# Kernel optimization log

Measured on AMD Instinct MI355X. Metric: run time of the kernel, lower is better.

## Reference

```python
import jax, jax.numpy as jnp
import numpy as np

VOC, EDIM, HDIM, SSZ, SDIM, SDEPTH, PAD = 32000, 256, 256, 128, 128, 2, 0
N, BSZ = 64, 32
T = 2 * N - 1  # 127
N_ACTS = 2  # push, pop


def _linear(key, out_d, in_d):
    k1, k2 = jax.random.split(key)
    return (jax.random.normal(k1, (out_d, in_d), jnp.float32) * 0.02,
            jax.random.normal(k2, (out_d,), jnp.float32) * 0.02)


def setup_inputs() -> dict:
    key = jax.random.key(0)
    ks = jax.random.split(key, 9)
    emb_W = jax.random.normal(ks[0], (VOC, EDIM), jnp.float32) * 0.02
    emb_W = emb_W.at[PAD].set(0.0)  # padding_idx row is zero in torch
    W_e2h, b_e2h = _linear(ks[1], HDIM, EDIM)
    W_s2h, b_s2h = _linear(ks[2], HDIM, SDIM * SDEPTH)
    W_h2h, b_h2h = _linear(ks[3], HDIM, HDIM)
    W_h2i, b_h2i = _linear(ks[4], N_ACTS + 1, HDIM)
    W_h2s, b_h2s = _linear(ks[5], SDIM, HDIM)
    W_s2u, b_s2u = _linear(ks[6], SDIM, SDIM * SDEPTH)
    empty_elem = jax.random.normal(ks[7], (1, SDIM), jnp.float32) * 0.02
    inputs = jax.random.randint(ks[8], (N, BSZ), 0, VOC)
    return dict(inputs=inputs, emb_W=emb_W, W_e2h=W_e2h, b_e2h=b_e2h,
                W_s2h=W_s2h, b_s2h=b_s2h, W_h2h=W_h2h, b_h2h=b_h2h,
                W_h2i=W_h2i, b_h2i=b_h2i, W_h2s=W_h2s, b_h2s=b_h2s,
                W_s2u=W_s2u, b_s2u=b_s2u, empty_elem=empty_elem)


def _srnn(inputs, emb_W, W_e2h, b_e2h, W_s2h, b_s2h, W_h2h, b_h2h,
          W_h2i, b_h2i, W_h2s, b_h2s, W_s2u, b_s2u, empty_elem):
    bsz = inputs.shape[1]
    embs = emb_W[inputs]                                        # [N, bsz, edim]
    pads = jnp.broadcast_to(emb_W[PAD], (T - N, bsz, EDIM))     # padded tail
    buf0 = jnp.concatenate([embs, pads], axis=0)                # [T, bsz, edim]
    hid0 = jnp.zeros((bsz, HDIM), jnp.float32)
    stack0 = jnp.broadcast_to(empty_elem, (bsz, SSZ, SDIM))

    def step(carry, t):
        hid, stack, buf = carry
        tops = stack[:, :SDEPTH, :].reshape(bsz, SDEPTH * SDIM)
        inp = buf[t]                                            # [bsz, edim]
        ihid = inp @ W_e2h.T + b_e2h + tops @ W_s2h.T + b_s2h
        hid = jax.nn.relu(hid @ W_h2h.T + b_h2h + ihid)
        inst = ihid @ W_h2i.T + b_h2i                           # [bsz, 3]
        act = jax.nn.softmax(inst[:, :N_ACTS], axis=-1)
        gamma = 1.0 + jnp.log1p(jnp.exp(inst[:, N_ACTS:]))      # [bsz, 1]
        a = act ** gamma
        a = a / (jnp.sum(a, axis=-1, keepdims=True) + 1e-16)    # sharpened acts
        p_push, p_pop = a[:, :1], a[:, 1:]                      # [bsz, 1]
        # buffer update: pop shifts the whole buffer down one slot along time
        buf_pop = jnp.concatenate([jnp.zeros_like(buf[:1]), buf[:-1]], axis=0)
        buf = p_push[None] * buf + p_pop[None] * buf_pop        # [1,bsz,1] bcast
        push_val = jax.nn.relu(hid @ W_h2s.T + b_h2s)           # [bsz, sdim]
        u_val = jax.nn.relu(tops @ W_s2u.T + b_s2u)             # [bsz, sdim]
        z = jnp.zeros((bsz, 1, SDIM), jnp.float32)
        # W_push (shift down by 1) as an index roll
        stack_push = jnp.concatenate([z, stack[:, :-1, :]], axis=1)
        stack_push = stack_push.at[:, 0, :].add(push_val)
        # W_pop = shift up by SDEPTH, then W_push = shift down by 1
        up = jnp.concatenate([stack[:, SDEPTH:, :],
                              jnp.zeros((bsz, SDEPTH, SDIM), jnp.float32)], axis=1)
        stack_pop = jnp.concatenate([z, up[:, :-1, :]], axis=1)
        stack_pop = stack_pop.at[:, 0, :].add(u_val)
        stack_pop = stack_pop.at[:, SSZ - SDEPTH + 1:, :].add(empty_elem[0])
        stack = p_push[:, :, None] * stack_push + p_pop[:, :, None] * stack_pop
        return (hid, stack, buf), (hid, a, stack[:, 0, :])

    (hid, stack, _), (outputs, acts, top_elems) = jax.lax.scan(
        step, (hid0, stack0, buf0), jnp.arange(T))
    return outputs, hid, stack, acts, top_elems


def reference(inputs, emb_W, W_e2h, b_e2h, W_s2h, b_s2h, W_h2h, b_h2h,
              W_h2i, b_h2i, W_h2s, b_h2s, W_s2u, b_s2u, empty_elem):
    return _srnn(inputs, emb_W, W_e2h, b_e2h, W_s2h, b_s2h, W_h2h, b_h2h,
                 W_h2i, b_h2i, W_h2s, b_h2s, W_s2u, b_s2u, empty_elem)
```

## Files before the change

kernel.cpp:

```cpp
#include <hip/hip_runtime.h>
#include <stdint.h>
#include <math.h>


#define T_STEPS 127

#define OUT_OFF   0
#define HID_OFF   1040384
#define STACK_OFF 1048576
#define ACTS_OFF  1572864
#define TE_OFF    1580992

#define E2H_OFF_U 131072

typedef _Float16 h2 __attribute__((ext_vector_type(2)));

__device__ __forceinline__ unsigned packh2(float a, float b){
  h2 v; v.x = (_Float16)a; v.y = (_Float16)b;
  return __builtin_bit_cast(unsigned, v);
}
__device__ __forceinline__ float h2loF(unsigned u){ h2 v = __builtin_bit_cast(h2,u); return (float)v.x; }
__device__ __forceinline__ float h2hiF(unsigned u){ h2 v = __builtin_bit_cast(h2,u); return (float)v.y; }

#if __has_builtin(__builtin_amdgcn_fdot2)
__device__ __forceinline__ float fdot2(unsigned a, unsigned b, float c){
  return __builtin_amdgcn_fdot2(__builtin_bit_cast(h2,a), __builtin_bit_cast(h2,b), c, false);
}
#else
__device__ __forceinline__ float fdot2(unsigned a, unsigned b, float c){
  return c + h2loF(a)*h2loF(b) + h2hiF(a)*h2hiF(b);
}
#endif

#define CHOFF(u) (12*((u)>>3) + ((u)&7))

__global__ void prep_pack(const float* __restrict__ We2h, const float* __restrict__ Ws2h,
                          const float* __restrict__ Wh2h, const float* __restrict__ Wh2s,
                          const float* __restrict__ Ws2u, uint4* __restrict__ out4){
  int gid = blockIdx.x*256 + threadIdx.x;
  const float* src;
  if (gid < 16384){
    int i = gid >> 10, t_ = gid & 1023;
    const float* S = (t_ < 512) ? Ws2h : Wh2h;
    int r = t_ & 511, jp = r >> 2, ks = r & 3;
    int j = 2*jp + (i >> 3);
    int k0 = ks*64 + (i & 7)*8;
    src = S + j*256 + k0;
  } else if (gid < 20480){
    int l = gid - 16384, i = l >> 10, t_ = l & 1023;
    int jr = t_ >> 4, kb = t_ & 15;
    int j = 2*jr + (i >> 1);
    int k0 = kb*16 + (i & 1)*8;
    src = Wh2s + j*256 + k0;
  } else if (gid < 24576){
    int l = gid - 20480, i = l >> 10, t_ = l & 1023;
    int jr = t_ >> 4, kb = t_ & 15;
    int j = 2*jr + (i >> 1);
    int k0 = kb*16 + (i & 1)*8;
    src = Ws2u + j*256 + k0;
  } else {
    int l = gid - 24576;
    int i8 = l >> 8, j = l & 255;
    src = We2h + j*256 + i8*8;
  }
  uint4 r4;
  r4.x = packh2(src[0], src[1]); r4.y = packh2(src[2], src[3]);
  r4.z = packh2(src[4], src[5]); r4.w = packh2(src[6], src[7]);
  out4[gid] = r4;
}

__global__ void prep_e2h(const int* __restrict__ inputs, const float* __restrict__ embW,
                         const uint4* __restrict__ w04, unsigned* __restrict__ e2hpk){
  __shared__ float emb[8][256];
  int tid = threadIdx.x;
  int r2 = blockIdx.x >> 3, bg = blockIdx.x & 7;
  for (int q=0;q<8;q++){
    int rr = q >> 2, bb = q & 3;
    int tok = inputs[(2*r2+rr)*32 + bg*4+bb];
    emb[q][tid] = embW[tok*256 + tid];
  }
  __syncthreads();
  float acc[8] = {0.f,0.f,0.f,0.f,0.f,0.f,0.f,0.f};
  for (int i8=0;i8<32;i8++){
    uint4 u = w04[i8*256 + tid];
    unsigned uu[4] = {u.x,u.y,u.z,u.w};
    #pragma unroll
    for (int c=0;c<4;c++){
      float lo = h2loF(uu[c]), hi = h2hiF(uu[c]);
      int k = i8*8 + c*2;
      #pragma unroll
      for (int q=0;q<8;q++)
        acc[q] += emb[q][k]*lo + emb[q][k+1]*hi;
    }
  }
  int base = (bg*4)*8192 + r2*256 + tid;
  #pragma unroll
  for (int bb=0;bb<4;bb++)
    e2hpk[base + bb*8192] = packh2(acc[bb], acc[4+bb]);
}

__global__ __attribute__((amdgpu_flat_work_group_size(1024,1024), amdgpu_waves_per_eu(4,4)))
void srnn_main(const uint4* __restrict__ ws4, const unsigned* __restrict__ wsu,
               const float* __restrict__ b_e2h, const float* __restrict__ b_s2h,
               const float* __restrict__ b_h2h, const float* __restrict__ Wh2i,
               const float* __restrict__ b_h2i, const float* __restrict__ b_h2s,
               const float* __restrict__ b_s2u, const float* __restrict__ empty_el,
               float* __restrict__ out)
{
  __shared__ __align__(16) float    stk_s[128*128];
  __shared__ __align__(16) unsigned e2h_s[32*258];
  __shared__ __align__(16) unsigned s_pk[192];
  __shared__ __align__(16) unsigned hid_pk[192];
  __shared__ __align__(16) float    pv_s[128], uv_s[128];
  __shared__ __align__(16) float    accih[256], acchp[256];
  __shared__ __align__(16) float    emptyf_s[128];
  __shared__ float    wbuf[2][192];
  __shared__ unsigned pkwc[32];
  __shared__ float    partsum[12];
  __shared__ float    pp_s, pq_s;

  const int tid = threadIdx.x;
  const int b   = blockIdx.x;
  const int aside = tid >> 9;
  const int ar  = tid & 511;
  const int ajp = ar >> 2;
  const int aks = ar & 3;
  const int jr  = tid >> 4;
  const int ksb = tid & 15;
  const int g   = tid >> 6;
  const int cp  = tid & 63;

  uint4 w1r[16], w3r[4], w2r[4];
  #pragma unroll
  for (int i=0;i<16;i++) w1r[i] = ws4[i*1024 + tid];
  #pragma unroll
  for (int i=0;i<4;i++)  w3r[i] = ws4[16384 + i*1024 + tid];
  #pragma unroll
  for (int i=0;i<4;i++)  w2r[i] = ws4[20480 + i*1024 + tid];

  float bA0=0.f, bA1=0.f;
  if (aks==0){
    int j0 = 2*ajp;
    if (aside==0){ bA0 = b_e2h[j0]+b_s2h[j0]; bA1 = b_e2h[j0+1]+b_s2h[j0+1]; }
    else         { bA0 = b_h2h[j0];           bA1 = b_h2h[j0+1]; }
  }
  float bH0=0.f,bH1=0.f,bU0=0.f,bU1=0.f;
  if (ksb==0){ bH0=b_h2s[2*jr]; bH1=b_h2s[2*jr+1]; bU0=b_s2u[2*jr]; bU1=b_s2u[2*jr+1]; }
  float rW0=0.f,rW1=0.f,rW2=0.f;
  if (tid<256){ rW0=Wh2i[tid]; rW1=Wh2i[256+tid]; rW2=Wh2i[512+tid]; }
  const float bi0=b_h2i[0], bi1=b_h2i[1], bi2=b_h2i[2];

  const unsigned* e2hg = wsu + E2H_OFF_U + b*8192;
  #pragma unroll
  for (int q=0;q<8;q++){
    int idx = q*1024 + tid;
    e2h_s[(idx>>8)*258 + (idx&255)] = e2hg[idx];
  }
  {
    float2 e2 = *(const float2*)&empty_el[2*cp];
    #pragma unroll
    for (int j=0;j<8;j++)
      *(float2*)&stk_s[(8*g+j)*128 + 2*cp] = e2;
  }
  if (tid < 128){
    emptyf_s[tid] = empty_el[tid];
    hid_pk[CHOFF(tid)] = 0u;
    int cu = tid & 63;
    s_pk[CHOFF(tid)] = packh2(empty_el[2*cu], empty_el[2*cu+1]);
  }
  if (tid < 192){ wbuf[0][tid] = (tid==64)?1.f:0.f; wbuf[1][tid]=0.f; }
  if (tid < 32)  pkwc[tid] = (tid==0)? packh2(1.f,0.f) : 0u;
  __syncthreads();

  int cur = 0;
  for (int t=0;t<T_STEPS;++t){
    {
      const unsigned* act  = aside ? hid_pk : s_pk;
      const unsigned* actB = act + 48*aks;
      float x0 = 0.f, x1 = 0.f;
      if (aside==0){
        #pragma unroll
        for (int q=0;q<8;q++){
          int r2 = aks*8 + q;
          unsigned cw = pkwc[r2];
          uint2 e = *(const uint2*)&e2h_s[r2*258 + 2*ajp];
          x0 = fdot2(cw, e.x, x0);
          x1 = fdot2(cw, e.y, x1);
        }
      }
      #pragma unroll
      for (int i=0;i<8;i++){
        uint4 A  = *(const uint4*)(actB + 12*(i>>1) + 4*(i&1));
        uint4 Wa = w1r[i], Wb = w1r[8+i];
        x0 = fdot2(A.x,Wa.x,x0); x0 = fdot2(A.y,Wa.y,x0);
        x0 = fdot2(A.z,Wa.z,x0); x0 = fdot2(A.w,Wa.w,x0);
        x1 = fdot2(A.x,Wb.x,x1); x1 = fdot2(A.y,Wb.y,x1);
        x1 = fdot2(A.z,Wb.z,x1); x1 = fdot2(A.w,Wb.w,x1);
      }
      x0 += __shfl_xor(x0,1); x0 += __shfl_xor(x0,2);
      x1 += __shfl_xor(x1,1); x1 += __shfl_xor(x1,2);
      if (aks==0){
        float* dst = aside ? acchp : accih;
        *(float2*)&dst[2*ajp] = make_float2(x0 + bA0, x1 + bA1);
      }
    }
    __syncthreads();

    if (tid < 128){
      float2 ih2 = *(const float2*)&accih[2*tid];
      float2 hp2 = *(const float2*)&acchp[2*tid];
      float hn0 = fmaxf(ih2.x+hp2.x, 0.f);
      float hn1 = fmaxf(ih2.y+hp2.y, 0.f);
      hid_pk[CHOFF(tid)] = packh2(hn0,hn1);
      *(float2*)&out[OUT_OFF + t*8192 + b*256 + 2*tid] = make_float2(hn0,hn1);
      if (t==T_STEPS-1) *(float2*)&out[HID_OFF + b*256 + 2*tid] = make_float2(hn0,hn1);
    }
    if (tid < 256){
      float v = accih[tid];
      float p0=v*rW0, p1=v*rW1, p2=v*rW2;
      #pragma unroll
      for (int o=32;o>=1;o>>=1){ p0+=__shfl_xor(p0,o); p1+=__shfl_xor(p1,o); p2+=__shfl_xor(p2,o); }
      if ((tid&63)==0){ int w=tid>>6; partsum[w*3]=p0; partsum[w*3+1]=p1; partsum[w*3+2]=p2; }
    }
    __syncthreads();

    if (tid < 64){
      float i0 = bi0+partsum[0]+partsum[3]+partsum[6]+partsum[9];
      float i1 = bi1+partsum[1]+partsum[4]+partsum[7]+partsum[10];
      float gi = bi2+partsum[2]+partsum[5]+partsum[8]+partsum[11];
      float mx = fmaxf(i0,i1);
      float e0 = expf(i0-mx), e1 = expf(i1-mx);
      float inv = 1.f/(e0+e1);
      float act0 = e0*inv, act1 = e1*inv;
      float gamma = 1.f + log1pf(expf(gi));
      float A0 = powf(act0,gamma), A1 = powf(act1,gamma);
      float sden = A0+A1+1e-16f;
      float ppv = A0/sden, pqv = A1/sden;
      if (tid==0){
        pp_s = ppv; pq_s = pqv;
        *(float2*)&out[ACTS_OFF + t*64 + b*2] = make_float2(ppv,pqv);
      }
    }

    {
      const uint4* hptr = (const uint4*)(hid_pk + 12*ksb);
      const uint4* sptr = (const uint4*)(s_pk   + 12*ksb);
      uint4 H0 = hptr[0], H1 = hptr[1];
      uint4 S0 = sptr[0], S1 = sptr[1];
      float h0=0.f,h1=0.f,u0=0.f,u1=0.f;
      h0=fdot2(H0.x,w3r[0].x,h0); h0=fdot2(H0.y,w3r[0].y,h0); h0=fdot2(H0.z,w3r[0].z,h0); h0=fdot2(H0.w,w3r[0].w,h0);
      h0=fdot2(H1.x,w3r[1].x,h0); h0=fdot2(H1.y,w3r[1].y,h0); h0=fdot2(H1.z,w3r[1].z,h0); h0=fdot2(H1.w,w3r[1].w,h0);
      h1=fdot2(H0.x,w3r[2].x,h1); h1=fdot2(H0.y,w3r[2].y,h1); h1=fdot2(H0.z,w3r[2].z,h1); h1=fdot2(H0.w,w3r[2].w,h1);
      h1=fdot2(H1.x,w3r[3].x,h1); h1=fdot2(H1.y,w3r[3].y,h1); h1=fdot2(H1.z,w3r[3].z,h1); h1=fdot2(H1.w,w3r[3].w,h1);
      u0=fdot2(S0.x,w2r[0].x,u0); u0=fdot2(S0.y,w2r[0].y,u0); u0=fdot2(S0.z,w2r[0].z,u0); u0=fdot2(S0.w,w2r[0].w,u0);
      u0=fdot2(S1.x,w2r[1].x,u0); u0=fdot2(S1.y,w2r[1].y,u0); u0=fdot2(S1.z,w2r[1].z,u0); u0=fdot2(S1.w,w2r[1].w,u0);
      u1=fdot2(S0.x,w2r[2].x,u1); u1=fdot2(S0.y,w2r[2].y,u1); u1=fdot2(S0.z,w2r[2].z,u1); u1=fdot2(S0.w,w2r[2].w,u1);
      u1=fdot2(S1.x,w2r[3].x,u1); u1=fdot2(S1.y,w2r[3].y,u1); u1=fdot2(S1.z,w2r[3].z,u1); u1=fdot2(S1.w,w2r[3].w,u1);
      #pragma unroll
      for (int o=8;o>=1;o>>=1){
        h0+=__shfl_xor(h0,o); h1+=__shfl_xor(h1,o);
        u0+=__shfl_xor(u0,o); u1+=__shfl_xor(u1,o);
      }
      if (ksb==0){
        pv_s[2*jr]   = fmaxf(h0+bH0,0.f);
        pv_s[2*jr+1] = fmaxf(h1+bH1,0.f);
        uv_s[2*jr]   = fmaxf(u0+bU0,0.f);
        uv_s[2*jr+1] = fmaxf(u1+bU1,0.f);
      }
    }
    __syncthreads();
    const float pp = pp_s, pq = pq_s;

    {
      float2 w[10];
      #pragma unroll
      for (int k=0;k<10;k++){
        int r = 8*g - 1 + k;
        if (r >= 0 && r <= 127)
          w[k] = *(const float2*)&stk_s[r*128 + 2*cp];
      }
      if (g == 15) w[9] = *(const float2*)&emptyf_s[2*cp];
      float2 pv2 = make_float2(0.f,0.f), uv2 = make_float2(0.f,0.f);
      if (g == 0){ pv2 = *(const float2*)&pv_s[2*cp]; uv2 = *(const float2*)&uv_s[2*cp]; }
      float2 nn[8];
      #pragma unroll
      for (int j=0;j<8;j++){
        nn[j].x = pp*w[j].x + pq*w[j+2].x;
        nn[j].y = pp*w[j].y + pq*w[j+2].y;
      }
      if (g == 0){
        nn[0].x = pp*pv2.x + pq*uv2.x;
        nn[0].y = pp*pv2.y + pq*uv2.y;
      }
      if (tid < 128){
        int k = 64+tid;
        wbuf[cur^1][k] = pp*wbuf[cur][k] + pq*wbuf[cur][k-1];
      } else if (tid < 160){
        int r2 = tid-128;
        int k1 = 65 + t - 2*r2;
        float wa = wbuf[cur][k1], wb2 = wbuf[cur][k1-1], wc2 = wbuf[cur][k1-2];
        pkwc[r2] = packh2(pp*wa+pq*wb2, pp*wb2+pq*wc2);
      }
      __syncthreads();
      #pragma unroll
      for (int j=0;j<8;j++)
        *(float2*)&stk_s[(8*g+j)*128 + 2*cp] = nn[j];
      if (g == 0){
        *(float2*)&out[TE_OFF + t*4096 + b*128 + 2*cp] = nn[0];
        s_pk[CHOFF(cp)]      = packh2(nn[0].x, nn[0].y);
        s_pk[CHOFF(64+cp)]   = packh2(nn[1].x, nn[1].y);
      }
    }
    __syncthreads();
    cur ^= 1;
  }

  #pragma unroll
  for (int j=0;j<8;j++){
    int r = 8*g + j;
    *(float2*)&out[STACK_OFF + b*16384 + r*128 + 2*cp] =
      *(const float2*)&stk_s[r*128 + 2*cp];
  }
}

extern "C" void kernel_launch(void* const* d_in, const int* in_sizes, int n_in,
                              void* d_out, int out_size, void* d_ws, size_t ws_size,
                              hipStream_t stream){
  const int*   inputs = (const int*)d_in[0];
  const float* embW   = (const float*)d_in[1];
  const float* We2h   = (const float*)d_in[2];
  const float* b_e2h  = (const float*)d_in[3];
  const float* Ws2h   = (const float*)d_in[4];
  const float* b_s2h  = (const float*)d_in[5];
  const float* Wh2h   = (const float*)d_in[6];
  const float* b_h2h  = (const float*)d_in[7];
  const float* Wh2i   = (const float*)d_in[8];
  const float* b_h2i  = (const float*)d_in[9];
  const float* Wh2s   = (const float*)d_in[10];
  const float* b_h2s  = (const float*)d_in[11];
  const float* Ws2u   = (const float*)d_in[12];
  const float* b_s2u  = (const float*)d_in[13];
  const float* empty  = (const float*)d_in[14];
  unsigned* wsu = (unsigned*)d_ws;

  prep_pack<<<dim3(128), dim3(256), 0, stream>>>(We2h, Ws2h, Wh2h, Wh2s, Ws2u, (uint4*)wsu);
  prep_e2h<<<dim3(256), dim3(256), 0, stream>>>(inputs, embW, ((const uint4*)wsu)+24576, wsu + E2H_OFF_U);
  srnn_main<<<dim3(32), dim3(1024), 0, stream>>>((const uint4*)wsu, (const unsigned*)wsu,
                                                 b_e2h, b_s2h, b_h2h, Wh2i, b_h2i,
                                                 b_h2s, b_s2u, empty, (float*)d_out);
}
```

Measured before the change: 892.0 us.

## Cut per-step barriers via halo double-buffering and fused stack projections

Merges the two prep kernels into one launch, with the e2h projection reading fp32 We2h directly. In the recurrent loop, the stack update now writes in place by keeping double-buffered halo rows for the rows just above and below each group. This removes the barrier between reading and writing the stack. The h2s/s2u projections are split across two halves of the block and use the freshly computed hidden state directly from the pre-activation sums. That lets them run in the same phase as the hidden update and removes another barrier per step. The trade-offs are more shared memory, some redundant relu/pack work, and a more complex indexing scheme.

```diff
diff --git a/kernel.cpp b/kernel.cpp
--- a/kernel.cpp
+++ b/kernel.cpp
@@ -11,6 +11,8 @@
 #define ACTS_OFF  1572864
 #define TE_OFF    1580992
 
+#define W3_OFF 16384
+#define W2_OFF 20480
 #define E2H_OFF_U 131072
 
 typedef _Float16 h2 __attribute__((ext_vector_type(2)));
@@ -33,47 +35,42 @@
 #endif
 
 #define CHOFF(u) (12*((u)>>3) + ((u)&7))
-
-__global__ void prep_pack(const float* __restrict__ We2h, const float* __restrict__ Ws2h,
-                          const float* __restrict__ Wh2h, const float* __restrict__ Wh2s,
-                          const float* __restrict__ Ws2u, uint4* __restrict__ out4){
-  int gid = blockIdx.x*256 + threadIdx.x;
-  const float* src;
-  if (gid < 16384){
-    int i = gid >> 10, t_ = gid & 1023;
-    const float* S = (t_ < 512) ? Ws2h : Wh2h;
-    int r = t_ & 511, jp = r >> 2, ks = r & 3;
-    int j = 2*jp + (i >> 3);
-    int k0 = ks*64 + (i & 7)*8;
-    src = S + j*256 + k0;
-  } else if (gid < 20480){
-    int l = gid - 16384, i = l >> 10, t_ = l & 1023;
-    int jr = t_ >> 4, kb = t_ & 15;
-    int j = 2*jr + (i >> 1);
-    int k0 = kb*16 + (i & 1)*8;
-    src = Wh2s + j*256 + k0;
-  } else if (gid < 24576){
-    int l = gid - 20480, i = l >> 10, t_ = l & 1023;
-    int jr = t_ >> 4, kb = t_ & 15;
-    int j = 2*jr + (i >> 1);
-    int k0 = kb*16 + (i & 1)*8;
-    src = Ws2u + j*256 + k0;
-  } else {
-    int l = gid - 24576;
-    int i8 = l >> 8, j = l & 255;
-    src = We2h + j*256 + i8*8;
-  }
-  uint4 r4;
-  r4.x = packh2(src[0], src[1]); r4.y = packh2(src[2], src[3]);
-  r4.z = packh2(src[4], src[5]); r4.w = packh2(src[6], src[7]);
-  out4[gid] = r4;
-}
-
-__global__ void prep_e2h(const int* __restrict__ inputs, const float* __restrict__ embW,
-                         const uint4* __restrict__ w04, unsigned* __restrict__ e2hpk){
+#define STGP(p)  (20*((p)>>3) + 2*((p)&7))
+
+__global__ void prep_all(const int* __restrict__ inputs, const float* __restrict__ embW,
+                         const float* __restrict__ We2h,
+                         const float* __restrict__ Ws2h, const float* __restrict__ Wh2h,
+                         const float* __restrict__ Wh2s, const float* __restrict__ Ws2u,
+                         uint4* __restrict__ out4, unsigned* __restrict__ e2hpk){
+  int tid = threadIdx.x;
+  int bi  = blockIdx.x;
+  if (bi >= 256){
+    int gid = (bi-256)*256 + tid;
+    const float* src;
+    if (gid < 16384){
+      int i = gid >> 10, t_ = gid & 1023;
+      const float* S = (t_ < 512) ? Ws2h : Wh2h;
+      int r = t_ & 511, jp = r >> 2, ks = r & 3;
+      int j  = 2*jp + (i >> 3);
+      int k0 = ks*64 + (i & 7)*8;
+      src = S + j*256 + k0;
+    } else {
+      int l = gid - 16384;
+      int region = l >> 12, li = l & 4095;
+      int i = li >> 9, rB = li & 511;
+      int jp = rB >> 3, ks = rB & 7;
+      int j  = 2*jp + (i >> 2);
+      int k0 = ks*32 + (i & 3)*8;
+      src = (region ? Ws2u : Wh2s) + j*256 + k0;
+    }
+    uint4 r4;
+    r4.x = packh2(src[0], src[1]); r4.y = packh2(src[2], src[3]);
+    r4.z = packh2(src[4], src[5]); r4.w = packh2(src[6], src[7]);
+    out4[gid] = r4;
+    return;
+  }
   __shared__ float emb[8][256];
-  int tid = threadIdx.x;
-  int r2 = blockIdx.x >> 3, bg = blockIdx.x & 7;
+  int r2 = bi >> 3, bg = bi & 7;
   for (int q=0;q<8;q++){
     int rr = q >> 2, bb = q & 3;
     int tok = inputs[(2*r2+rr)*32 + bg*4+bb];
@@ -82,11 +79,12 @@
   __syncthreads();
   float acc[8] = {0.f,0.f,0.f,0.f,0.f,0.f,0.f,0.f};
   for (int i8=0;i8<32;i8++){
-    uint4 u = w04[i8*256 + tid];
-    unsigned uu[4] = {u.x,u.y,u.z,u.w};
+    float4 f0 = *(const float4*)&We2h[tid*256 + i8*8];
+    float4 f1 = *(const float4*)&We2h[tid*256 + i8*8 + 4];
+    float wv[8] = {f0.x,f0.y,f0.z,f0.w,f1.x,f1.y,f1.z,f1.w};
     #pragma unroll
     for (int c=0;c<4;c++){
-      float lo = h2loF(uu[c]), hi = h2hiF(uu[c]);
+      float lo = wv[2*c], hi = wv[2*c+1];
       int k = i8*8 + c*2;
       #pragma unroll
       for (int q=0;q<8;q++)
@@ -108,15 +106,15 @@
                float* __restrict__ out)
 {
   __shared__ __align__(16) float    stk_s[128*128];
-  __shared__ __align__(16) unsigned e2h_s[32*258];
-  __shared__ __align__(16) unsigned s_pk[192];
-  __shared__ __align__(16) unsigned hid_pk[192];
+  __shared__ __align__(16) unsigned e2h4[16*520];
+  __shared__ __align__(16) float    halo_top[2][16*128];
+  __shared__ __align__(16) float    halo_bot[2][16*128];
+  __shared__ __align__(16) float    accih_st[320], acchp_st[320];
+  __shared__ __align__(16) unsigned s_pk[192], hid_pk[192];
   __shared__ __align__(16) float    pv_s[128], uv_s[128];
-  __shared__ __align__(16) float    accih[256], acchp[256];
-  __shared__ __align__(16) float    emptyf_s[128];
+  __shared__ __align__(16) float    whi_s[768];
   __shared__ float    wbuf[2][192];
   __shared__ unsigned pkwc[32];
-  __shared__ float    partsum[12];
   __shared__ float    pp_s, pq_s;
 
   const int tid = threadIdx.x;
@@ -125,18 +123,21 @@
   const int ar  = tid & 511;
   const int ajp = ar >> 2;
   const int aks = ar & 3;
-  const int jr  = tid >> 4;
-  const int ksb = tid & 15;
+  const int rB  = tid & 511;
+  const int jpB = rB >> 3;
+  const int ksB = rB & 7;
+  const int h2sSide = (tid >= 512);
   const int g   = tid >> 6;
   const int cp  = tid & 63;
 
-  uint4 w1r[16], w3r[4], w2r[4];
+  uint4 w1r[16], wBr[8];
   #pragma unroll
   for (int i=0;i<16;i++) w1r[i] = ws4[i*1024 + tid];
-  #pragma unroll
-  for (int i=0;i<4;i++)  w3r[i] = ws4[16384 + i*1024 + tid];
-  #pragma unroll
-  for (int i=0;i<4;i++)  w2r[i] = ws4[20480 + i*1024 + tid];
+  {
+    int wbase = h2sSide ? W3_OFF : W2_OFF;
+    #pragma unroll
+    for (int i=0;i<8;i++) wBr[i] = ws4[wbase + i*512 + rB];
+  }
 
   float bA0=0.f, bA1=0.f;
   if (aks==0){
@@ -144,26 +145,28 @@
     if (aside==0){ bA0 = b_e2h[j0]+b_s2h[j0]; bA1 = b_e2h[j0+1]+b_s2h[j0+1]; }
     else         { bA0 = b_h2h[j0];           bA1 = b_h2h[j0+1]; }
   }
-  float bH0=0.f,bH1=0.f,bU0=0.f,bU1=0.f;
-  if (ksb==0){ bH0=b_h2s[2*jr]; bH1=b_h2s[2*jr+1]; bU0=b_s2u[2*jr]; bU1=b_s2u[2*jr+1]; }
-  float rW0=0.f,rW1=0.f,rW2=0.f;
-  if (tid<256){ rW0=Wh2i[tid]; rW1=Wh2i[256+tid]; rW2=Wh2i[512+tid]; }
+  float bB0=0.f, bB1=0.f;
+  if (ksB==0){
+    const float* bb = h2sSide ? b_h2s : b_s2u;
+    bB0 = bb[2*jpB]; bB1 = bb[2*jpB+1];
+  }
   const float bi0=b_h2i[0], bi1=b_h2i[1], bi2=b_h2i[2];
 
   const unsigned* e2hg = wsu + E2H_OFF_U + b*8192;
   #pragma unroll
   for (int q=0;q<8;q++){
     int idx = q*1024 + tid;
-    e2h_s[(idx>>8)*258 + (idx&255)] = e2hg[idx];
-  }
-  {
-    float2 e2 = *(const float2*)&empty_el[2*cp];
-    #pragma unroll
-    for (int j=0;j<8;j++)
-      *(float2*)&stk_s[(8*g+j)*128 + 2*cp] = e2;
-  }
+    int r2 = idx >> 8, j = idx & 255;
+    e2h4[(r2>>1)*520 + 2*j + (r2&1)] = e2hg[idx];
+  }
+  const float2 emt2 = *(const float2*)&empty_el[2*cp];
+  #pragma unroll
+  for (int j=0;j<8;j++)
+    *(float2*)&stk_s[(8*g+j)*128 + 2*cp] = emt2;
+  *(float2*)&halo_top[0][g*128 + 2*cp] = emt2;
+  *(float2*)&halo_bot[0][g*128 + 2*cp] = emt2;
+  if (tid < 768) whi_s[tid] = Wh2i[tid];
   if (tid < 128){
-    emptyf_s[tid] = empty_el[tid];
     hid_pk[CHOFF(tid)] = 0u;
     int cu = tid & 63;
     s_pk[CHOFF(tid)] = packh2(empty_el[2*cu], empty_el[2*cu+1]);
@@ -180,12 +183,13 @@
       float x0 = 0.f, x1 = 0.f;
       if (aside==0){
         #pragma unroll
-        for (int q=0;q<8;q++){
-          int r2 = aks*8 + q;
-          unsigned cw = pkwc[r2];
-          uint2 e = *(const uint2*)&e2h_s[r2*258 + 2*ajp];
-          x0 = fdot2(cw, e.x, x0);
-          x1 = fdot2(cw, e.y, x1);
+        for (int qq=0;qq<4;qq++){
+          int r2g = 4*aks + qq;
+          unsigned cwE = pkwc[8*aks + 2*qq];
+          unsigned cwO = pkwc[8*aks + 2*qq + 1];
+          uint4 u = *(const uint4*)&e2h4[r2g*520 + 4*ajp];
+          x0 = fdot2(cwE, u.x, x0); x0 = fdot2(cwO, u.y, x0);
+          x1 = fdot2(cwE, u.z, x1); x1 = fdot2(cwO, u.w, x1);
         }
       }
       #pragma unroll
@@ -200,34 +204,70 @@
       x0 += __shfl_xor(x0,1); x0 += __shfl_xor(x0,2);
       x1 += __shfl_xor(x1,1); x1 += __shfl_xor(x1,2);
       if (aks==0){
-        float* dst = aside ? acchp : accih;
-        *(float2*)&dst[2*ajp] = make_float2(x0 + bA0, x1 + bA1);
+        float* dst = aside ? acchp_st : accih_st;
+        *(float2*)&dst[STGP(ajp)] = make_float2(x0 + bA0, x1 + bA1);
       }
     }
     __syncthreads();
 
-    if (tid < 128){
-      float2 ih2 = *(const float2*)&accih[2*tid];
-      float2 hp2 = *(const float2*)&acchp[2*tid];
+    if (tid >= 64 && tid < 192){
+      int hl = tid - 64;
+      int w_ = STGP(hl);
+      float2 ih2 = *(const float2*)&accih_st[w_];
+      float2 hp2 = *(const float2*)&acchp_st[w_];
       float hn0 = fmaxf(ih2.x+hp2.x, 0.f);
       float hn1 = fmaxf(ih2.y+hp2.y, 0.f);
-      hid_pk[CHOFF(tid)] = packh2(hn0,hn1);
-      *(float2*)&out[OUT_OFF + t*8192 + b*256 + 2*tid] = make_float2(hn0,hn1);
-      if (t==T_STEPS-1) *(float2*)&out[HID_OFF + b*256 + 2*tid] = make_float2(hn0,hn1);
-    }
-    if (tid < 256){
-      float v = accih[tid];
-      float p0=v*rW0, p1=v*rW1, p2=v*rW2;
-      #pragma unroll
-      for (int o=32;o>=1;o>>=1){ p0+=__shfl_xor(p0,o); p1+=__shfl_xor(p1,o); p2+=__shfl_xor(p2,o); }
-      if ((tid&63)==0){ int w=tid>>6; partsum[w*3]=p0; partsum[w*3+1]=p1; partsum[w*3+2]=p2; }
-    }
-    __syncthreads();
+      hid_pk[CHOFF(hl)] = packh2(hn0,hn1);
+      *(float2*)&out[OUT_OFF + t*8192 + b*256 + 2*hl] = make_float2(hn0,hn1);
+      if (t==T_STEPS-1) *(float2*)&out[HID_OFF + b*256 + 2*hl] = make_float2(hn0,hn1);
+    }
+
+    {
+      float y0=0.f, y1=0.f;
+      #pragma unroll
+      for (int i=0;i<4;i++){
+        unsigned u0,u1,u2,u3;
+        if (h2sSide){
+          const int off = 40*ksB + ((i>=2)?20:0) + 8*(i&1);
+          float4 a0 = *(const float4*)(accih_st + off);
+          float4 a1 = *(const float4*)(accih_st + off + 4);
+          float4 c0 = *(const float4*)(acchp_st + off);
+          float4 c1 = *(const float4*)(acchp_st + off + 4);
+          u0 = packh2(fmaxf(a0.x+c0.x,0.f), fmaxf(a0.y+c0.y,0.f));
+          u1 = packh2(fmaxf(a0.z+c0.z,0.f), fmaxf(a0.w+c0.w,0.f));
+          u2 = packh2(fmaxf(a1.x+c1.x,0.f), fmaxf(a1.y+c1.y,0.f));
+          u3 = packh2(fmaxf(a1.z+c1.z,0.f), fmaxf(a1.w+c1.w,0.f));
+        } else {
+          uint4 S = *(const uint4*)&s_pk[12*(2*ksB + (i>>1)) + 4*(i&1)];
+          u0 = S.x; u1 = S.y; u2 = S.z; u3 = S.w;
+        }
+        uint4 Wa = wBr[i], Wb = wBr[4+i];
+        y0=fdot2(u0,Wa.x,y0); y0=fdot2(u1,Wa.y,y0); y0=fdot2(u2,Wa.z,y0); y0=fdot2(u3,Wa.w,y0);
+        y1=fdot2(u0,Wb.x,y1); y1=fdot2(u1,Wb.y,y1); y1=fdot2(u2,Wb.z,y1); y1=fdot2(u3,Wb.w,y1);
+      }
+      y0 += __shfl_xor(y0,1); y0 += __shfl_xor(y0,2); y0 += __shfl_xor(y0,4);
+      y1 += __shfl_xor(y1,1); y1 += __shfl_xor(y1,2); y1 += __shfl_xor(y1,4);
+      if (ksB==0){
+        float* dst = h2sSide ? pv_s : uv_s;
+        dst[2*jpB]   = fmaxf(y0+bB0,0.f);
+        dst[2*jpB+1] = fmaxf(y1+bB1,0.f);
+      }
+    }
 
     if (tid < 64){
-      float i0 = bi0+partsum[0]+partsum[3]+partsum[6]+partsum[9];
-      float i1 = bi1+partsum[1]+partsum[4]+partsum[7]+partsum[10];
-      float gi = bi2+partsum[2]+partsum[5]+partsum[8]+partsum[11];
+      int l = tid;
+      float4 av = *(const float4*)&accih_st[20*(l>>2) + 4*(l&3)];
+      float4 q0 = *(const float4*)&whi_s[4*l];
+      float4 q1 = *(const float4*)&whi_s[256 + 4*l];
+      float4 q2 = *(const float4*)&whi_s[512 + 4*l];
+      float p0 = av.x*q0.x + av.y*q0.y + av.z*q0.z + av.w*q0.w;
+      float p1 = av.x*q1.x + av.y*q1.y + av.z*q1.z + av.w*q1.w;
+      float p2 = av.x*q2.x + av.y*q2.y + av.z*q2.z + av.w*q2.w;
+      #pragma unroll
+      for (int o=1;o<=32;o<<=1){
+        p0 += __shfl_xor(p0,o); p1 += __shfl_xor(p1,o); p2 += __shfl_xor(p2,o);
+      }
+      float i0 = bi0+p0, i1 = bi1+p1, gi = bi2+p2;
       float mx = fmaxf(i0,i1);
       float e0 = expf(i0-mx), e1 = expf(i1-mx);
       float inv = 1.f/(e0+e1);
@@ -235,62 +275,45 @@
       float gamma = 1.f + log1pf(expf(gi));
       float A0 = powf(act0,gamma), A1 = powf(act1,gamma);
       float sden = A0+A1+1e-16f;
-      float ppv = A0/sden, pqv = A1/sden;
-      if (tid==0){
+      if (l==0){
+        float ppv = A0/sden, pqv = A1/sden;
         pp_s = ppv; pq_s = pqv;
         *(float2*)&out[ACTS_OFF + t*64 + b*2] = make_float2(ppv,pqv);
       }
     }
-
-    {
-      const uint4* hptr = (const uint4*)(hid_pk + 12*ksb);
-      const uint4* sptr = (const uint4*)(s_pk   + 12*ksb);
-      uint4 H0 = hptr[0], H1 = hptr[1];
-      uint4 S0 = sptr[0], S1 = sptr[1];
-      float h0=0.f,h1=0.f,u0=0.f,u1=0.f;
-      h0=fdot2(H0.x,w3r[0].x,h0); h0=fdot2(H0.y,w3r[0].y,h0); h0=fdot2(H0.z,w3r[0].z,h0); h0=fdot2(H0.w,w3r[0].w,h0);
-      h0=fdot2(H1.x,w3r[1].x,h0); h0=fdot2(H1.y,w3r[1].y,h0); h0=fdot2(H1.z,w3r[1].z,h0); h0=fdot2(H1.w,w3r[1].w,h0);
-      h1=fdot2(H0.x,w3r[2].x,h1); h1=fdot2(H0.y,w3r[2].y,h1); h1=fdot2(H0.z,w3r[2].z,h1); h1=fdot2(H0.w,w3r[2].w,h1);
-      h1=fdot2(H1.x,w3r[3].x,h1); h1=fdot2(H1.y,w3r[3].y,h1); h1=fdot2(H1.z,w3r[3].z,h1); h1=fdot2(H1.w,w3r[3].w,h1);
-      u0=fdot2(S0.x,w2r[0].x,u0); u0=fdot2(S0.y,w2r[0].y,u0); u0=fdot2(S0.z,w2r[0].z,u0); u0=fdot2(S0.w,w2r[0].w,u0);
-      u0=fdot2(S1.x,w2r[1].x,u0); u0=fdot2(S1.y,w2r[1].y,u0); u0=fdot2(S1.z,w2r[1].z,u0); u0=fdot2(S1.w,w2r[1].w,u0);
-      u1=fdot2(S0.x,w2r[2].x,u1); u1=fdot2(S0.y,w2r[2].y,u1); u1=fdot2(S0.z,w2r[2].z,u1); u1=fdot2(S0.w,w2r[2].w,u1);
-      u1=fdot2(S1.x,w2r[3].x,u1); u1=fdot2(S1.y,w2r[3].y,u1); u1=fdot2(S1.z,w2r[3].z,u1); u1=fdot2(S1.w,w2r[3].w,u1);
-      #pragma unroll
-      for (int o=8;o>=1;o>>=1){
-        h0+=__shfl_xor(h0,o); h1+=__shfl_xor(h1,o);
-        u0+=__shfl_xor(u0,o); u1+=__shfl_xor(u1,o);
-      }
-      if (ksb==0){
-        pv_s[2*jr]   = fmaxf(h0+bH0,0.f);
-        pv_s[2*jr+1] = fmaxf(h1+bH1,0.f);
-        uv_s[2*jr]   = fmaxf(u0+bU0,0.f);
-        uv_s[2*jr+1] = fmaxf(u1+bU1,0.f);
-      }
-    }
     __syncthreads();
     const float pp = pp_s, pq = pq_s;
 
     {
       float2 w[10];
       #pragma unroll
-      for (int k=0;k<10;k++){
-        int r = 8*g - 1 + k;
-        if (r >= 0 && r <= 127)
-          w[k] = *(const float2*)&stk_s[r*128 + 2*cp];
-      }
-      if (g == 15) w[9] = *(const float2*)&emptyf_s[2*cp];
+      for (int k=1;k<=8;k++)
+        w[k] = *(const float2*)&stk_s[(8*g + k - 1)*128 + 2*cp];
+      w[0] = (g>0)  ? *(const float2*)&halo_bot[cur][(g-1)*128 + 2*cp]
+                    : make_float2(0.f,0.f);
+      w[9] = (g<15) ? *(const float2*)&halo_top[cur][(g+1)*128 + 2*cp]
+                    : emt2;
       float2 pv2 = make_float2(0.f,0.f), uv2 = make_float2(0.f,0.f);
       if (g == 0){ pv2 = *(const float2*)&pv_s[2*cp]; uv2 = *(const float2*)&uv_s[2*cp]; }
-      float2 nn[8];
+      float2 nn0, nn1;
       #pragma unroll
       for (int j=0;j<8;j++){
-        nn[j].x = pp*w[j].x + pq*w[j+2].x;
-        nn[j].y = pp*w[j].y + pq*w[j+2].y;
+        float2 nv;
+        nv.x = pp*w[j].x + pq*w[j+2].x;
+        nv.y = pp*w[j].y + pq*w[j+2].y;
+        if (j==0 && g==0){
+          nv.x = pp*pv2.x + pq*uv2.x;
+          nv.y = pp*pv2.y + pq*uv2.y;
+        }
+        *(float2*)&stk_s[(8*g+j)*128 + 2*cp] = nv;
+        if (j==0){ nn0 = nv; *(float2*)&halo_top[cur^1][g*128 + 2*cp] = nv; }
+        if (j==1){ nn1 = nv; }
+        if (j==7){ *(float2*)&halo_bot[cur^1][g*128 + 2*cp] = nv; }
       }
       if (g == 0){
-        nn[0].x = pp*pv2.x + pq*uv2.x;
-        nn[0].y = pp*pv2.y + pq*uv2.y;
+        *(float2*)&out[TE_OFF + t*4096 + b*128 + 2*cp] = nn0;
+        s_pk[CHOFF(cp)]    = packh2(nn0.x, nn0.y);
+        s_pk[CHOFF(64+cp)] = packh2(nn1.x, nn1.y);
       }
       if (tid < 128){
         int k = 64+tid;
@@ -301,26 +324,15 @@
         float wa = wbuf[cur][k1], wb2 = wbuf[cur][k1-1], wc2 = wbuf[cur][k1-2];
         pkwc[r2] = packh2(pp*wa+pq*wb2, pp*wb2+pq*wc2);
       }
-      __syncthreads();
-      #pragma unroll
-      for (int j=0;j<8;j++)
-        *(float2*)&stk_s[(8*g+j)*128 + 2*cp] = nn[j];
-      if (g == 0){
-        *(float2*)&out[TE_OFF + t*4096 + b*128 + 2*cp] = nn[0];
-        s_pk[CHOFF(cp)]      = packh2(nn[0].x, nn[0].y);
-        s_pk[CHOFF(64+cp)]   = packh2(nn[1].x, nn[1].y);
-      }
     }
     __syncthreads();
     cur ^= 1;
   }
 
   #pragma unroll
-  for (int j=0;j<8;j++){
-    int r = 8*g + j;
-    *(float2*)&out[STACK_OFF + b*16384 + r*128 + 2*cp] =
-      *(const float2*)&stk_s[r*128 + 2*cp];
-  }
+  for (int j=0;j<8;j++)
+    *(float2*)&out[STACK_OFF + b*16384 + (8*g+j)*128 + 2*cp] =
+      *(const float2*)&stk_s[(8*g+j)*128 + 2*cp];
 }
 
 extern "C" void kernel_launch(void* const* d_in, const int* in_sizes, int n_in,
@@ -343,8 +355,9 @@
   const float* empty  = (const float*)d_in[14];
   unsigned* wsu = (unsigned*)d_ws;
 
-  prep_pack<<<dim3(128), dim3(256), 0, stream>>>(We2h, Ws2h, Wh2h, Wh2s, Ws2u, (uint4*)wsu);
-  prep_e2h<<<dim3(256), dim3(256), 0, stream>>>(inputs, embW, ((const uint4*)wsu)+24576, wsu + E2H_OFF_U);
+  prep_all<<<dim3(352), dim3(256), 0, stream>>>(inputs, embW, We2h, Ws2h, Wh2h,
+                                                Wh2s, Ws2u, (uint4*)wsu,
+                                                wsu + E2H_OFF_U);
   srnn_main<<<dim3(32), dim3(1024), 0, stream>>>((const uint4*)wsu, (const unsigned*)wsu,
                                                  b_e2h, b_s2h, b_h2h, Wh2i, b_h2i,
                                                  b_h2s, b_s2u, empty, (float*)d_out);
```

Measured after the change: 891.4 us. Within noise of the previous version (-0.1%).
